# Kernel tuning notes

Hardware: AMD Instinct MI355X
Metric: run time of the kernel (lower is better)

## Reference

```python
import jax, jax.numpy as jnp
import numpy as np

N, IN, OUT = 8192, 4096, 4096
GROUP = 4
ACT_BITS = 8


def setup_inputs() -> dict:
    key = jax.random.key(0)
    k_x, k_w, k_b = jax.random.split(key, 3)
    input = jax.random.normal(k_x, (N, IN), dtype=jnp.float32)
    # ternary weights in {-1, 0, +1}, stored as float for compute
    weight = jax.random.randint(k_w, (OUT, IN), -1, 2).astype(jnp.float32)
    weight_scale = jnp.ones((1,), dtype=jnp.float32) * 0.02
    bias = jax.random.normal(k_b, (OUT,), dtype=jnp.float32) * 0.01
    return {"input": input, "weight": weight, "weight_scale": weight_scale, "bias": bias}


def reference(input, weight, weight_scale, bias):
    n, in_f = input.shape
    out_f = weight.shape[0]
    qmax = 2 ** (ACT_BITS - 1) - 1  # 127
    # absmax activation quantization (inference path)
    act_scale = jnp.abs(input).max() / qmax
    x_q = jnp.clip(jnp.round(input / act_scale), -(qmax + 1), qmax)
    # LUT path math: per 4-wide group, contribution = sum(w_group) * mean(x_group)
    g = in_f // GROUP
    x_mean = x_q.reshape(n, g, GROUP).mean(axis=-1)          # [N, G]
    w_sum = weight.reshape(out_f, g, GROUP).sum(axis=-1)     # [OUT, G]
    out = jnp.einsum('ng,og->no', x_mean, w_sum)
    out = out * weight_scale * act_scale + bias
    return out
```

## Files before the change

### kernel.cpp

```cpp
#include <hip/hip_runtime.h>
#include <hip/hip_bf16.h>

#define NROWS 8192
#define INF   4096
#define OUTF  4096
#define G     1024

typedef _Float16 f16x8 __attribute__((ext_vector_type(8)));
typedef float    f32x4 __attribute__((ext_vector_type(4)));

__global__ void absmax_kernel(const float4* __restrict__ x, int n4,
                              unsigned int* __restrict__ out_bits) {
    float m = 0.f;
    for (int i = blockIdx.x * blockDim.x + threadIdx.x; i < n4;
         i += gridDim.x * blockDim.x) {
        float4 v = x[i];
        m = fmaxf(m, fmaxf(fmaxf(fabsf(v.x), fabsf(v.y)),
                           fmaxf(fabsf(v.z), fabsf(v.w))));
    }
    for (int off = 32; off; off >>= 1)
        m = fmaxf(m, __shfl_down(m, off));
    __shared__ float wm[4];
    int lane = threadIdx.x & 63, wave = threadIdx.x >> 6;
    if (lane == 0) wm[wave] = m;
    __syncthreads();
    if (threadIdx.x == 0) {
        float bm = fmaxf(fmaxf(wm[0], wm[1]), fmaxf(wm[2], wm[3]));
        atomicMax(out_bits, __float_as_uint(bm));
    }
}

__global__ void quant_kernel(const float4* __restrict__ x,
                             _Float16* __restrict__ xs,
                             const unsigned int* __restrict__ max_bits,
                             int ngroups) {
    int i = blockIdx.x * blockDim.x + threadIdx.x;
    if (i >= ngroups) return;
    float s = __uint_as_float(*max_bits) * (1.0f / 127.0f);
    float4 v = x[i];
    float q0 = fminf(fmaxf(rintf(v.x / s), -128.f), 127.f);
    float q1 = fminf(fmaxf(rintf(v.y / s), -128.f), 127.f);
    float q2 = fminf(fmaxf(rintf(v.z / s), -128.f), 127.f);
    float q3 = fminf(fmaxf(rintf(v.w / s), -128.f), 127.f);
    xs[i] = (_Float16)(q0 + q1 + q2 + q3);
}

__global__ void wsum_kernel(const float4* __restrict__ w,
                            _Float16* __restrict__ ws,
                            int ngroups) {
    int i = blockIdx.x * blockDim.x + threadIdx.x;
    if (i >= ngroups) return;
    float4 v = w[i];
    ws[i] = (_Float16)(v.x + v.y + v.z + v.w);
}

#define TILE 128
#define BK   32

__device__ __forceinline__ void async_copy16(const void* g, void* l) {
    __builtin_amdgcn_global_load_lds(
        (const __attribute__((address_space(1))) unsigned int*)g,
        (__attribute__((address_space(3))) unsigned int*)l,
        16, 0, 0);
}

__global__ __launch_bounds__(256, 2) void gemm_kernel(
    const _Float16* __restrict__ A,
    const _Float16* __restrict__ B,
    const float* __restrict__ bias,
    const unsigned int* __restrict__ max_bits,
    const float* __restrict__ wscale,
    float* __restrict__ out) {

    __shared__ alignas(16) _Float16 As[TILE * BK];
    __shared__ alignas(16) _Float16 Bs[TILE * BK];

    const int t = threadIdx.x;
    const int lane = t & 63;
    const int wave = t >> 6;
    const int wm = (wave >> 1) * 64;
    const int wn = (wave & 1) * 64;

    const long rowA0 = (long)blockIdx.y * TILE;
    const long rowB0 = (long)blockIdx.x * TILE;

    f32x4 acc[4][4] = {};

    const int srow = (lane >> 2);
    const int scol = (lane & 3) * 8;

    for (int k0 = 0; k0 < G; k0 += BK) {
        __syncthreads();
        #pragma unroll
        for (int i = 0; i < 2; ++i) {
            const int c = wave + i * 4;
            const int row = c * 16 + srow;
            const _Float16* ga = A + (rowA0 + row) * (long)G + k0 + scol;
            const _Float16* gb = B + (rowB0 + row) * (long)G + k0 + scol;
            async_copy16(ga, As + c * 512);
            async_copy16(gb, Bs + c * 512);
        }
        __syncthreads();

        f16x8 af[4], bf[4];
        #pragma unroll
        for (int mi = 0; mi < 4; ++mi)
            af[mi] = *(const f16x8*)&As[(wm + mi * 16 + (lane & 15)) * BK + (lane >> 4) * 8];
        #pragma unroll
        for (int nj = 0; nj < 4; ++nj)
            bf[nj] = *(const f16x8*)&Bs[(wn + nj * 16 + (lane & 15)) * BK + (lane >> 4) * 8];

        #pragma unroll
        for (int mi = 0; mi < 4; ++mi)
            #pragma unroll
            for (int nj = 0; nj < 4; ++nj)
                acc[mi][nj] = __builtin_amdgcn_mfma_f32_16x16x32_f16(
                    af[mi], bf[nj], acc[mi][nj], 0, 0, 0);
    }

    const float scale = __uint_as_float(*max_bits) * (0.25f / 127.0f) * wscale[0];
    const int r0 = (int)rowA0 + wm + (lane >> 4) * 4;
    const int c0 = (int)rowB0 + wn + (lane & 15);
    #pragma unroll
    for (int nj = 0; nj < 4; ++nj) {
        const int col = c0 + nj * 16;
        const float b = bias[col];
        #pragma unroll
        for (int mi = 0; mi < 4; ++mi) {
            const int row = r0 + mi * 16;
            #pragma unroll
            for (int r = 0; r < 4; ++r)
                out[(long)(row + r) * OUTF + col] = acc[mi][nj][r] * scale + b;
        }
    }
}

extern "C" void kernel_launch(void* const* d_in, const int* in_sizes, int n_in,
                              void* d_out, int out_size, void* d_ws, size_t ws_size,
                              hipStream_t stream) {
    const float* input  = (const float*)d_in[0];
    const float* weight = (const float*)d_in[1];
    const float* wscale = (const float*)d_in[2];
    const float* bias   = (const float*)d_in[3];
    float* out = (float*)d_out;

    unsigned int* max_bits = (unsigned int*)d_ws;
    _Float16* x_sum = (_Float16*)((char*)d_ws + 256);
    _Float16* w_sum = (_Float16*)((char*)d_ws + 256 + (size_t)NROWS * G * 2);

    hipMemsetAsync(d_ws, 0, 4, stream);

    absmax_kernel<<<2048, 256, 0, stream>>>(
        (const float4*)input, NROWS * INF / 4, max_bits);

    quant_kernel<<<(NROWS * G + 255) / 256, 256, 0, stream>>>(
        (const float4*)input, x_sum, max_bits, NROWS * G);

    wsum_kernel<<<(OUTF * G + 255) / 256, 256, 0, stream>>>(
        (const float4*)weight, w_sum, OUTF * G);

    gemm_kernel<<<dim3(OUTF / TILE, NROWS / TILE), 256, 0, stream>>>(
        x_sum, w_sum, bias, max_bits, wscale, out);
}
```

Before: 385.1 us.

## Enlarge GEMM tile, split absmax into two passes, fuse quant and wsum kernels

The GEMM block tile grows from 128x128 to 256x128, so each wave holds an 8x4 MFMA accumulator grid. This is meant to improve operand reuse from LDS and halve the number of A-tile reloads per output. The atomic absmax plus memset is replaced by a fixed-grid partial-max kernel followed by a single-block final reduction that writes the precomputed scale. The quant and weight-sum kernels are merged into one launch. Together these cut launch count and per-element division setup, at the cost of higher register pressure in the GEMM (128 accumulator floats per lane under launch_bounds 256,2), which may spill or lower occupancy.

```diff
diff --git a/kernel.cpp b/kernel.cpp
--- a/kernel.cpp
+++ b/kernel.cpp
@@ -9,11 +9,14 @@
 typedef _Float16 f16x8 __attribute__((ext_vector_type(8)));
 typedef float    f32x4 __attribute__((ext_vector_type(4)));
 
-__global__ void absmax_kernel(const float4* __restrict__ x, int n4,
-                              unsigned int* __restrict__ out_bits) {
+
+__global__ void absmax_part(const float4* __restrict__ x,
+                            float* __restrict__ partial) {
+    const int stride = 1024 * 256;
+    int i = blockIdx.x * 256 + threadIdx.x;
     float m = 0.f;
-    for (int i = blockIdx.x * blockDim.x + threadIdx.x; i < n4;
-         i += gridDim.x * blockDim.x) {
+    #pragma unroll 4
+    for (int it = 0; it < 32; ++it, i += stride) {
         float4 v = x[i];
         m = fmaxf(m, fmaxf(fmaxf(fabsf(v.x), fabsf(v.y)),
                            fmaxf(fabsf(v.z), fabsf(v.w))));
@@ -24,38 +27,61 @@
     int lane = threadIdx.x & 63, wave = threadIdx.x >> 6;
     if (lane == 0) wm[wave] = m;
     __syncthreads();
-    if (threadIdx.x == 0) {
+    if (threadIdx.x == 0)
+        partial[blockIdx.x] = fmaxf(fmaxf(wm[0], wm[1]), fmaxf(wm[2], wm[3]));
+}
+
+__global__ void absmax_final(const float* __restrict__ partial,
+                             float* __restrict__ scale_out) {
+    int t = threadIdx.x;
+    float m = fmaxf(fmaxf(partial[t], partial[t + 256]),
+                    fmaxf(partial[t + 512], partial[t + 768]));
+    for (int off = 32; off; off >>= 1)
+        m = fmaxf(m, __shfl_down(m, off));
+    __shared__ float wm[4];
+    int lane = t & 63, wave = t >> 6;
+    if (lane == 0) wm[wave] = m;
+    __syncthreads();
+    if (t == 0) {
         float bm = fmaxf(fmaxf(wm[0], wm[1]), fmaxf(wm[2], wm[3]));
-        atomicMax(out_bits, __float_as_uint(bm));
+        scale_out[0] = bm * (1.0f / 127.0f);
     }
 }
 
-__global__ void quant_kernel(const float4* __restrict__ x,
-                             _Float16* __restrict__ xs,
-                             const unsigned int* __restrict__ max_bits,
-                             int ngroups) {
-    int i = blockIdx.x * blockDim.x + threadIdx.x;
-    if (i >= ngroups) return;
-    float s = __uint_as_float(*max_bits) * (1.0f / 127.0f);
-    float4 v = x[i];
-    float q0 = fminf(fmaxf(rintf(v.x / s), -128.f), 127.f);
-    float q1 = fminf(fmaxf(rintf(v.y / s), -128.f), 127.f);
-    float q2 = fminf(fmaxf(rintf(v.z / s), -128.f), 127.f);
-    float q3 = fminf(fmaxf(rintf(v.w / s), -128.f), 127.f);
-    xs[i] = (_Float16)(q0 + q1 + q2 + q3);
+__global__ void prep_fused(const float4* __restrict__ x,
+                           const float4* __restrict__ w,
+                           const float* __restrict__ scale_p,
+                           _Float16* __restrict__ xs,
+                           _Float16* __restrict__ ws) {
+    const int b = blockIdx.x;
+    const int t = threadIdx.x;
+    if (b < 16384) {
+        const float s = scale_p[0];
+        int i0 = b * 512 + t;
+        #pragma unroll
+        for (int u = 0; u < 2; ++u) {
+            int i = i0 + u * 256;
+            float4 v = x[i];
+            float q0 = fminf(fmaxf(rintf(v.x / s), -128.f), 127.f);
+            float q1 = fminf(fmaxf(rintf(v.y / s), -128.f), 127.f);
+            float q2 = fminf(fmaxf(rintf(v.z / s), -128.f), 127.f);
+            float q3 = fminf(fmaxf(rintf(v.w / s), -128.f), 127.f);
+            xs[i] = (_Float16)(q0 + q1 + q2 + q3);
+        }
+    } else {
+        int i0 = (b - 16384) * 512 + t;
+        #pragma unroll
+        for (int u = 0; u < 2; ++u) {
+            int i = i0 + u * 256;
+            float4 v = w[i];
+            ws[i] = (_Float16)(v.x + v.y + v.z + v.w);
+        }
+    }
 }
 
-__global__ void wsum_kernel(const float4* __restrict__ w,
-                            _Float16* __restrict__ ws,
-                            int ngroups) {
-    int i = blockIdx.x * blockDim.x + threadIdx.x;
-    if (i >= ngroups) return;
-    float4 v = w[i];
-    ws[i] = (_Float16)(v.x + v.y + v.z + v.w);
-}
-
-#define TILE 128
-#define BK   32
+#define BM 256
+#define BN 128
+#define BK 32
 
 __device__ __forceinline__ void async_copy16(const void* g, void* l) {
     __builtin_amdgcn_global_load_lds(
@@ -68,57 +94,59 @@
     const _Float16* __restrict__ A,
     const _Float16* __restrict__ B,
     const float* __restrict__ bias,
-    const unsigned int* __restrict__ max_bits,
+    const float* __restrict__ scale_p,
     const float* __restrict__ wscale,
     float* __restrict__ out) {
 
-    __shared__ alignas(16) _Float16 As[TILE * BK];
-    __shared__ alignas(16) _Float16 Bs[TILE * BK];
+    __shared__ alignas(16) _Float16 As[BM * BK];
+    __shared__ alignas(16) _Float16 Bs[BN * BK];
 
     const int t = threadIdx.x;
     const int lane = t & 63;
     const int wave = t >> 6;
-    const int wm = (wave >> 1) * 64;
+    const int wm = (wave >> 1) * 128;
     const int wn = (wave & 1) * 64;
 
-    const long rowA0 = (long)blockIdx.y * TILE;
-    const long rowB0 = (long)blockIdx.x * TILE;
+    const long rowA0 = (long)blockIdx.y * BM;
+    const long rowB0 = (long)blockIdx.x * BN;
 
-    f32x4 acc[4][4] = {};
+    f32x4 acc[8][4] = {};
 
-    const int srow = (lane >> 2);
+    const int srow = lane >> 2;
     const int scol = (lane & 3) * 8;
 
     for (int k0 = 0; k0 < G; k0 += BK) {
         __syncthreads();
         #pragma unroll
-        for (int i = 0; i < 2; ++i) {
-            const int c = wave + i * 4;
-            const int row = c * 16 + srow;
-            const _Float16* ga = A + (rowA0 + row) * (long)G + k0 + scol;
-            const _Float16* gb = B + (rowB0 + row) * (long)G + k0 + scol;
-            async_copy16(ga, As + c * 512);
-            async_copy16(gb, Bs + c * 512);
+        for (int i = 0; i < 6; ++i) {
+            const int c = wave * 6 + i;
+            if (c < 16) {
+                const int row = c * 16 + srow;
+                async_copy16(A + (rowA0 + row) * (long)G + k0 + scol, As + c * 512);
+            } else {
+                const int row = (c - 16) * 16 + srow;
+                async_copy16(B + (rowB0 + row) * (long)G + k0 + scol, Bs + (c - 16) * 512);
+            }
         }
         __syncthreads();
 
-        f16x8 af[4], bf[4];
+        f16x8 af[8], bf[4];
         #pragma unroll
-        for (int mi = 0; mi < 4; ++mi)
+        for (int mi = 0; mi < 8; ++mi)
             af[mi] = *(const f16x8*)&As[(wm + mi * 16 + (lane & 15)) * BK + (lane >> 4) * 8];
         #pragma unroll
         for (int nj = 0; nj < 4; ++nj)
             bf[nj] = *(const f16x8*)&Bs[(wn + nj * 16 + (lane & 15)) * BK + (lane >> 4) * 8];
 
         #pragma unroll
-        for (int mi = 0; mi < 4; ++mi)
+        for (int mi = 0; mi < 8; ++mi)
             #pragma unroll
             for (int nj = 0; nj < 4; ++nj)
                 acc[mi][nj] = __builtin_amdgcn_mfma_f32_16x16x32_f16(
                     af[mi], bf[nj], acc[mi][nj], 0, 0, 0);
     }
 
-    const float scale = __uint_as_float(*max_bits) * (0.25f / 127.0f) * wscale[0];
+    const float scale = scale_p[0] * 0.25f * wscale[0];
     const int r0 = (int)rowA0 + wm + (lane >> 4) * 4;
     const int c0 = (int)rowB0 + wn + (lane & 15);
     #pragma unroll
@@ -126,7 +154,7 @@
         const int col = c0 + nj * 16;
         const float b = bias[col];
         #pragma unroll
-        for (int mi = 0; mi < 4; ++mi) {
+        for (int mi = 0; mi < 8; ++mi) {
             const int row = r0 + mi * 16;
             #pragma unroll
             for (int r = 0; r < 4; ++r)
@@ -144,21 +172,15 @@
     const float* bias   = (const float*)d_in[3];
     float* out = (float*)d_out;
 
-    unsigned int* max_bits = (unsigned int*)d_ws;
-    _Float16* x_sum = (_Float16*)((char*)d_ws + 256);
-    _Float16* w_sum = (_Float16*)((char*)d_ws + 256 + (size_t)NROWS * G * 2);
+    float* act_scale = (float*)d_ws;
+    float* partials  = (float*)((char*)d_ws + 16);
+    _Float16* x_sum  = (_Float16*)((char*)d_ws + 8192);
+    _Float16* w_sum  = (_Float16*)((char*)d_ws + 8192 + (size_t)NROWS * G * 2);
 
-    hipMemsetAsync(d_ws, 0, 4, stream);
-
-    absmax_kernel<<<2048, 256, 0, stream>>>(
-        (const float4*)input, NROWS * INF / 4, max_bits);
-
-    quant_kernel<<<(NROWS * G + 255) / 256, 256, 0, stream>>>(
-        (const float4*)input, x_sum, max_bits, NROWS * G);
-
-    wsum_kernel<<<(OUTF * G + 255) / 256, 256, 0, stream>>>(
-        (const float4*)weight, w_sum, OUTF * G);
-
-    gemm_kernel<<<dim3(OUTF / TILE, NROWS / TILE), 256, 0, stream>>>(
-        x_sum, w_sum, bias, max_bits, wscale, out);
+    absmax_part<<<1024, 256, 0, stream>>>((const float4*)input, partials);
+    absmax_final<<<1, 256, 0, stream>>>(partials, act_scale);
+    prep_fused<<<24576, 256, 0, stream>>>((const float4*)input, (const float4*)weight,
+                                          act_scale, x_sum, w_sum);
+    gemm_kernel<<<dim3(OUTF / BN, NROWS / BM), 256, 0, stream>>>(
+        x_sum, w_sum, bias, act_scale, wscale, out);
 }
```

Result: faster. 376.1 us (-2.3%).
